# Kernel tuning notes

Measured on AMD Instinct MI355X. Metric: run time of the kernel, lower is better.

The kernel has to match this reference:

```python
import jax, jax.numpy as jnp
import numpy as np

NUM_ITEMS = 50000
EMBED = 256
HEADS = 8
HEAD_DIM = EMBED // HEADS
B, S = 32, 512
NEG_BIG = -1e9   # mask fill for dot-product scores
NEG_SMALL = -1e5 # mask fill for rel / time maps (as in RKT)


def setup_inputs() -> dict:
    key = jax.random.key(0)
    ks = jax.random.split(key, 20)
    sc = 0.02
    return {
        "item_inputs": jax.random.randint(ks[0], (B, S), 0, NUM_ITEMS + 1),
        "label_inputs": jax.random.randint(ks[1], (B, S), 0, 2, dtype=jnp.int32),
        "item_ids": jax.random.randint(ks[2], (B, S), 0, NUM_ITEMS + 1),
        "rel": jax.random.uniform(ks[3], (B, S, S), jnp.float32),
        "timestamp": jax.random.uniform(ks[4], (B, S, S), jnp.float32) * 10.0,
        # learned params
        "item_embeds": jax.random.normal(ks[5], (NUM_ITEMS + 1, EMBED), jnp.float32) * sc,
        "W_in": jax.random.normal(ks[6], (2 * EMBED, EMBED), jnp.float32) * sc,
        "b_in": jnp.zeros((EMBED,), jnp.float32),
        "Wq": jax.random.normal(ks[7], (EMBED, EMBED), jnp.float32) * sc,
        "bq": jnp.zeros((EMBED,), jnp.float32),
        "Wk": jax.random.normal(ks[8], (EMBED, EMBED), jnp.float32) * sc,
        "bk": jnp.zeros((EMBED,), jnp.float32),
        "Wv": jax.random.normal(ks[9], (EMBED, EMBED), jnp.float32) * sc,
        "bv": jnp.zeros((EMBED,), jnp.float32),
        "W_out": jax.random.normal(ks[10], (EMBED, 1), jnp.float32) * sc,
        "b_out": jnp.zeros((1,), jnp.float32),
        "l1": jnp.float32(0.5),
        "l2": jnp.float32(0.5),
    }


def _split_heads(t, W, b):
    # [B,S,E] -> [B,H,S,HD]
    return (t @ W + b).reshape(B, S, HEADS, HEAD_DIM).transpose(0, 2, 1, 3)


def reference(item_inputs, label_inputs, item_ids, rel, timestamp, item_embeds,
              W_in, b_in, Wq, bq, Wk, bk, Wv, bv, W_out, b_out, l1, l2):
    # --- input construction: response-gated duplicated item embedding ---
    e = item_embeds[item_inputs]                       # [B,S,E]
    lab = label_inputs[..., None].astype(e.dtype)      # [B,S,1]
    inputs = jnp.concatenate([e * lab, e * (1.0 - lab)], axis=-1)  # [B,S,2E]
    inputs = jax.nn.relu(inputs @ W_in + b_in)         # [B,S,E]
    query = item_embeds[item_ids]                      # [B,S,E]

    future = jnp.triu(jnp.ones((S, S), bool), 1)       # True above diagonal

    Q = _split_heads(query, Wq, bq)
    K = _split_heads(inputs, Wk, bk)
    V = _split_heads(inputs, Wv, bv)

    # scaled dot-product scores with causal mask
    scores = jnp.einsum('bhqd,bhkd->bhqk', Q, K) / np.float32(np.sqrt(HEAD_DIM))
    prob_attn = jax.nn.softmax(jnp.where(future, NEG_BIG, scores), axis=-1)

    # relational (item-item correlation) attention, future-masked
    rel_m = rel * (~future).astype(rel.dtype)          # [B,S,S]
    rel_attn = jax.nn.softmax(jnp.where(rel_m == 0, NEG_SMALL, rel_m), axis=-1)
    rel_attn = rel_attn[:, None]                       # broadcast over heads

    # exponential time-decay attention, future-masked
    ts = jnp.exp(-jnp.abs(timestamp))
    time_attn = jax.nn.softmax(jnp.where(future, NEG_SMALL, ts), axis=-1)[:, None]

    attn = (1.0 - l2) * prob_attn + l2 * time_attn
    attn = (1.0 - l1) * attn + l1 * rel_attn           # [B,H,S,S]

    out = jnp.einsum('bhqk,bhkd->bhqd', attn, V)       # [B,H,S,HD]
    out = out.transpose(0, 2, 1, 3).reshape(B, S, EMBED)
    logits = out @ W_out + b_out                       # [B,S,1]
    return logits, attn
```

## Files before the change

kernel.cpp:

```cpp
#include <hip/hip_runtime.h>
#include <hip/hip_bf16.h>

#define SEQ 512
#define EMB 256
#define NHEAD 8
#define HD 32

using bf16x8 = __attribute__((ext_vector_type(8))) short;
using f32x4  = __attribute__((ext_vector_type(4))) float;

static __device__ __forceinline__ unsigned short f2bf(float x) {
    union { float f; unsigned int u; } v; v.f = x;
    unsigned int r = v.u + 0x7FFFu + ((v.u >> 16) & 1u);
    return (unsigned short)(r >> 16);
}
static __device__ __forceinline__ float bf2f(unsigned short v) {
    union { unsigned int u; float f; } w; w.u = ((unsigned int)v) << 16; return w.f;
}

__global__ __launch_bounds__(256) void fused_prep_kernel(
    const int* __restrict__ item_inputs,
    const int* __restrict__ label_inputs,
    const int* __restrict__ item_ids,
    const float* __restrict__ embeds,
    const float* __restrict__ W_in,
    const float* __restrict__ Wq,
    const float* __restrict__ Wk,
    const float* __restrict__ Wv,
    const float* __restrict__ Wout,
    const float* __restrict__ bv,
    const float* __restrict__ bout,
    const float* __restrict__ rel,
    const float* __restrict__ tsp,
    unsigned short* __restrict__ Abig,
    unsigned short* __restrict__ qbf,
    unsigned short* __restrict__ WTin,
    unsigned short* __restrict__ WTq,
    unsigned short* __restrict__ WTk,
    float* __restrict__ Wvw,
    float* __restrict__ bvw,
    float* __restrict__ logits,
    float* __restrict__ denp,
    float* __restrict__ dent,
    float* __restrict__ denr)
{
    const int bid = blockIdx.x;
    const int t = threadIdx.x;

    if (bid < 4096) {
        int r = bid * 4 + (t >> 6);
        int j = (t & 63) * 4;
        int item = item_inputs[r];
        int lab  = label_inputs[r];
        int qid  = item_ids[r];
        float4 e4 = *(const float4*)(embeds + (size_t)item * EMB + j);
        ushort4 on  = make_ushort4(f2bf(e4.x), f2bf(e4.y), f2bf(e4.z), f2bf(e4.w));
        ushort4 off = make_ushort4(0, 0, 0, 0);
        *(ushort4*)(Abig + (size_t)r * 512 + j)       = lab ? on : off;
        *(ushort4*)(Abig + (size_t)r * 512 + 256 + j) = lab ? off : on;
        float4 q4 = *(const float4*)(embeds + (size_t)qid * EMB + j);
        *(ushort4*)(qbf + (size_t)r * 256 + j) =
            make_ushort4(f2bf(q4.x), f2bf(q4.y), f2bf(q4.z), f2bf(q4.w));
    } else if (bid < 5705) {
        int idx = (bid - 4096) * 256 + t;
        if (idx < 131072) {
            int n = idx >> 9, k = idx & 511;
            WTin[idx] = f2bf(W_in[(size_t)k * 256 + n]);
        } else if (idx < 196608) {
            int i = idx - 131072;
            int n = i >> 8, k = i & 255;
            WTq[i] = f2bf(Wq[(size_t)k * 256 + n]);
        } else if (idx < 262144) {
            int i = idx - 196608;
            int n = i >> 8, k = i & 255;
            WTk[i] = f2bf(Wk[(size_t)k * 256 + n]);
        } else if (idx < 264192) {
            int i = idx - 262144;
            int c = i >> 3, h = i & 7;
            float s = 0.f;
            #pragma unroll
            for (int d = 0; d < 32; d++)
                s += Wv[(size_t)c * 256 + h * 32 + d] * Wout[h * 32 + d];
            Wvw[i] = s;
        } else if (idx < 264200) {
            int h = idx - 264192;
            float s = 0.f;
            #pragma unroll
            for (int d = 0; d < 32; d++) s += bv[h * 32 + d] * Wout[h * 32 + d];
            bvw[h] = s;
        } else if (idx < 280584) {
            logits[idx - 264200] = bout[0];
        } else if (idx < 411656) {
            denp[idx - 280584] = 0.f;
        }
    } else {
        const int id2 = bid - 5705;
        const int b = id2 >> 4;
        const int qt = id2 & 15;
        const int q0 = qt * 32;
        const int row = t >> 3;
        const int lane8 = t & 7;
        const int qrow = q0 + row;
        const size_t base = ((size_t)(b * SEQ) + qrow) * SEQ;
        float dt = 0.f, dr = 0.f;
        for (int k4 = lane8 * 4; k4 <= qrow; k4 += 32) {
            float4 tv4 = *(const float4*)(tsp + base + k4);
            float4 rv4 = *(const float4*)(rel + base + k4);
            const float* tvp = &tv4.x;
            const float* rvp = &rv4.x;
            #pragma unroll
            for (int j = 0; j < 4; j++) {
                const bool va = (k4 + j) <= qrow;
                dt += va ? __expf(__expf(-fabsf(tvp[j]))) : 0.f;
                dr += (va && rvp[j] != 0.f) ? __expf(rvp[j]) : 0.f;
            }
        }
        dt += __shfl_xor(dt, 1); dt += __shfl_xor(dt, 2); dt += __shfl_xor(dt, 4);
        dr += __shfl_xor(dr, 1); dr += __shfl_xor(dr, 2); dr += __shfl_xor(dr, 4);
        if (lane8 == 0) {
            dent[b * SEQ + qrow] = dt;
            denr[b * SEQ + qrow] = dr;
        }
    }
}

template<int KDIM, int RELU, int OUTBF>
static __device__ __forceinline__ void gemm_body(
    const unsigned short* __restrict__ A,
    const unsigned short* __restrict__ BT,
    const float* __restrict__ bias,
    void* __restrict__ Cout, float scale)
{
    __shared__ unsigned short As[64][40];
    __shared__ unsigned short Bs[128][40];
    const int t = threadIdx.x;
    const int row0 = blockIdx.x * 64;
    const int col0 = blockIdx.y * 128;
    const int wid = t >> 6, lane = t & 63;
    const int wm = wid & 1, wn = wid >> 1;
    const int lg = lane >> 4, l15 = lane & 15;

    f32x4 acc[2][4];
    #pragma unroll
    for (int i = 0; i < 2; i++)
        #pragma unroll
        for (int j = 0; j < 4; j++) acc[i][j] = (f32x4){0.f, 0.f, 0.f, 0.f};

    const int arow = t >> 2, achk = t & 3;
    const int brow = t >> 1, bhalf = t & 1;

    for (int k0 = 0; k0 < KDIM; k0 += 32) {
        __syncthreads();
        *(uint4*)(&As[arow][achk * 8]) =
            *(const uint4*)(A + (size_t)(row0 + arow) * KDIM + k0 + achk * 8);
        const unsigned short* bsrc = BT + (size_t)(col0 + brow) * KDIM + k0 + bhalf * 16;
        *(uint4*)(&Bs[brow][bhalf * 16])     = *(const uint4*)(bsrc);
        *(uint4*)(&Bs[brow][bhalf * 16 + 8]) = *(const uint4*)(bsrc + 8);
        __syncthreads();
        bf16x8 af[2], bfr[4];
        #pragma unroll
        for (int fm = 0; fm < 2; fm++)
            af[fm] = *(const bf16x8*)(&As[wm * 32 + fm * 16 + l15][lg * 8]);
        #pragma unroll
        for (int fn = 0; fn < 4; fn++)
            bfr[fn] = *(const bf16x8*)(&Bs[wn * 64 + fn * 16 + l15][lg * 8]);
        #pragma unroll
        for (int fm = 0; fm < 2; fm++)
            #pragma unroll
            for (int fn = 0; fn < 4; fn++)
                acc[fm][fn] = __builtin_amdgcn_mfma_f32_16x16x32_bf16(
                    af[fm], bfr[fn], acc[fm][fn], 0, 0, 0);
    }
    #pragma unroll
    for (int fm = 0; fm < 2; fm++)
        #pragma unroll
        for (int fn = 0; fn < 4; fn++) {
            int col = col0 + wn * 64 + fn * 16 + l15;
            float bvv = bias[col];
            #pragma unroll
            for (int r = 0; r < 4; r++) {
                int row = row0 + wm * 32 + fm * 16 + lg * 4 + r;
                float v = acc[fm][fn][r] + bvv;
                if (RELU) v = fmaxf(v, 0.f);
                v *= scale;
                if (OUTBF) ((unsigned short*)Cout)[(size_t)row * 256 + col] = f2bf(v);
                else       ((float*)Cout)[(size_t)row * 256 + col] = v;
            }
        }
}

__global__ __launch_bounds__(256, 2) void gemmA_kernel(
    const unsigned short* __restrict__ Abig,
    const unsigned short* __restrict__ WTin,
    const float* __restrict__ b_in,
    unsigned short* __restrict__ Xbf,
    const unsigned short* __restrict__ qbf,
    const unsigned short* __restrict__ WTq,
    const float* __restrict__ bq,
    unsigned short* __restrict__ Qbf)
{
    if (blockIdx.z == 0)
        gemm_body<512, 1, 1>(Abig, WTin, b_in, (void*)Xbf, 1.0f);
    else
        gemm_body<256, 0, 1>(qbf, WTq, bq, (void*)Qbf, 0.17677669529663687f);
}

static __device__ __forceinline__ void vw_body(
    const unsigned short* __restrict__ Xbf,
    const float* __restrict__ Wvw,
    const float* __restrict__ bvw,
    float* __restrict__ Vw)
{
    __shared__ float sW[2048];
    __shared__ float sb[8];
    int t = threadIdx.x;
    #pragma unroll
    for (int i = 0; i < 8; i++) sW[i * 256 + t] = Wvw[i * 256 + t];
    if (t < 8) sb[t] = bvw[t];
    __syncthreads();
    int row = blockIdx.x * 256 + t;
    float acc[8];
    #pragma unroll
    for (int h = 0; h < 8; h++) acc[h] = sb[h];
    for (int d0 = 0; d0 < 32; d0++) {
        bf16x8 x = *(const bf16x8*)(Xbf + (size_t)row * 256 + d0 * 8);
        #pragma unroll
        for (int j = 0; j < 8; j++) {
            float xf = bf2f((unsigned short)x[j]);
            #pragma unroll
            for (int h = 0; h < 8; h++) acc[h] += xf * sW[(d0 * 8 + j) * 8 + h];
        }
    }
    *(float4*)(Vw + (size_t)row * 8)     = make_float4(acc[0], acc[1], acc[2], acc[3]);
    *(float4*)(Vw + (size_t)row * 8 + 4) = make_float4(acc[4], acc[5], acc[6], acc[7]);
}

__global__ __launch_bounds__(256, 2) void gemmB_kernel(
    const unsigned short* __restrict__ Xbf,
    const unsigned short* __restrict__ WTk,
    const float* __restrict__ bk,
    unsigned short* __restrict__ Kbf,
    const float* __restrict__ Wvw,
    const float* __restrict__ bvw,
    float* __restrict__ Vw)
{
    if (blockIdx.z == 0) {
        gemm_body<256, 0, 1>(Xbf, WTk, bk, (void*)Kbf, 1.0f);
    } else {
        if (blockIdx.x >= 64 || blockIdx.y != 0) return;
        vw_body(Xbf, Wvw, bvw, Vw);
    }
}

__global__ __launch_bounds__(256, 8) void attnDp_kernel(
    const unsigned short* __restrict__ Qbf,
    const unsigned short* __restrict__ Kbf,
    float* __restrict__ denp)
{
    const int t = threadIdx.x;
    const int id = blockIdx.x;
    const int b  = id >> 6;
    const int qt = (id >> 2) & 15;
    const int kc = id & 3;
    const int q0 = qt * 32;
    const int w = t >> 6, lane = t & 63;
    const int l15 = lane & 15, lg = lane >> 4;

    bf16x8 aq[2][2];
    #pragma unroll
    for (int hh = 0; hh < 2; hh++)
        #pragma unroll
        for (int mf = 0; mf < 2; mf++)
            aq[hh][mf] = *(const bf16x8*)(Qbf +
                (size_t)(b * SEQ + q0 + mf * 16 + l15) * EMB + (2 * w + hh) * 32 + lg * 8);

    float dp[2][2][4] = {};
    #pragma unroll 1
    for (int i = 0; i < 4; i++) {
        const int kt = kc + 4 * i;
        if (kt > qt) break;
        const int k0 = kt * 32;
        #pragma unroll
        for (int hh = 0; hh < 2; hh++) {
            #pragma unroll
            for (int nf = 0; nf < 2; nf++) {
                bf16x8 bk = *(const bf16x8*)(Kbf +
                    (size_t)(b * SEQ + k0 + nf * 16 + l15) * EMB + (2 * w + hh) * 32 + lg * 8);
                const int kcol = k0 + nf * 16 + l15;
                #pragma unroll
                for (int mf = 0; mf < 2; mf++) {
                    f32x4 am = __builtin_amdgcn_mfma_f32_16x16x32_bf16(
                        aq[hh][mf], bk, (f32x4){0, 0, 0, 0}, 0, 0, 0);
                    #pragma unroll
                    for (int r = 0; r < 4; r++) {
                        const int qrow = q0 + mf * 16 + lg * 4 + r;
                        dp[hh][mf][r] += (kcol <= qrow) ? __expf(am[r]) : 0.f;
                    }
                }
            }
        }
    }

    #pragma unroll
    for (int hh = 0; hh < 2; hh++)
        #pragma unroll
        for (int mf = 0; mf < 2; mf++)
            #pragma unroll
            for (int r = 0; r < 4; r++) {
                float v = dp[hh][mf][r];
                v += __shfl_xor(v, 1); v += __shfl_xor(v, 2);
                v += __shfl_xor(v, 4); v += __shfl_xor(v, 8);
                if (l15 == 0)
                    atomicAdd(&denp[((size_t)(b * NHEAD + 2 * w + hh)) * SEQ
                                    + q0 + mf * 16 + lg * 4 + r], v);
            }
}

__global__ __launch_bounds__(256, 8) void attnW_kernel(
    const unsigned short* __restrict__ Qbf,
    const unsigned short* __restrict__ Kbf,
    const float* __restrict__ Vw,
    const float* __restrict__ rel,
    const float* __restrict__ tsp,
    const float* __restrict__ denp,
    const float* __restrict__ dent,
    const float* __restrict__ denr,
    const float* __restrict__ pl1,
    const float* __restrict__ pl2,
    float* __restrict__ logits,
    float* __restrict__ attn)
{
    __shared__ float sT[16][260];
    __shared__ float slog[4][16];

    const int t = threadIdx.x;
    const int id = blockIdx.x;
    const int qt16 = 31 - (id >> 8);
    const int b = (id >> 3) & 31;
    const int h = id & 7;
    const int q0 = qt16 * 16;
    const int qmax = q0 + 15;

    const int w = t >> 6, lane = t & 63;
    const int l15 = lane & 15, lg = lane >> 4;

    const float l1 = pl1[0], l2 = pl2[0];
    const float cp = (1.f - l1) * (1.f - l2);
    const float ct = (1.f - l1) * l2;
    const float cr = l1;

    const int wrow = t >> 4;
    const int wcol = (t & 15) * 4;
    const int qrow_w = q0 + wrow;
    const float dtv = dent[b * SEQ + qrow_w];
    const float drv = denr[b * SEQ + qrow_w];
    const float ctt = ct / dtv;
    const float crr = drv > 0.f ? cr / drv : 0.f;

    float* arow_base = attn + ((size_t)((b * NHEAD + h) * SEQ) + q0 + wrow) * SEQ;
    const size_t rbase = ((size_t)(b * SEQ) + qrow_w) * SEQ;

    bf16x8 aq = *(const bf16x8*)(Qbf + (size_t)(b * SEQ + q0 + l15) * EMB + h * 32 + lg * 8);

    float invp[4];
    #pragma unroll
    for (int r = 0; r < 4; r++)
        invp[r] = 1.f / denp[((size_t)(b * NHEAD + h)) * SEQ + q0 + lg * 4 + r];

    float plog[4] = {0.f, 0.f, 0.f, 0.f};
    const f32x4 z4 = (f32x4){0.f, 0.f, 0.f, 0.f};

    for (int pass = 0; pass < 2; pass++) {
        const int c0 = pass * 256;
        if (c0 > qmax) {
            #pragma unroll
            for (int s = 0; s < 4; s++) {
                const int cf = wcol + s * 64;
                __builtin_nontemporal_store(z4, (f32x4*)(arow_base + c0 + cf));
            }
            continue;
        }
        #pragma unroll
        for (int s = 0; s < 4; s++) {
            const int cf = wcol + s * 64;
            const int kbase = c0 + cf;
            if (kbase > qrow_w) {
                *(f32x4*)(&sT[wrow][cf]) = z4;
            } else {
                float4 tv4 = *(const float4*)(tsp + rbase + kbase);
                float4 rv4 = *(const float4*)(rel + rbase + kbase);
                const float* tvp = &tv4.x;
                const float* rvp = &rv4.x;
                f32x4 o;
                #pragma unroll
                for (int j = 0; j < 4; j++) {
                    const bool va = (kbase + j) <= qrow_w;
                    float e_t = va ? __expf(__expf(-fabsf(tvp[j]))) * ctt : 0.f;
                    float e_r = (va && rvp[j] != 0.f) ? __expf(rvp[j]) * crr : 0.f;
                    o[j] = e_t + e_r;
                }
                *(f32x4*)(&sT[wrow][cf]) = o;
            }
        }
        __syncthreads();
        #pragma unroll
        for (int ki = 0; ki < 2; ki++) {
            const int kt = w + ki * 4;
            const int k0 = c0 + kt * 32;
            if (k0 <= qmax) {
                #pragma unroll
                for (int nf = 0; nf < 2; nf++) {
                    const int kcol = k0 + nf * 16 + l15;
                    const int lcol = kt * 32 + nf * 16 + l15;
                    bf16x8 bk = *(const bf16x8*)(Kbf +
                        (size_t)(b * SEQ + kcol) * EMB + h * 32 + lg * 8);
                    const float vwv = Vw[(size_t)(b * SEQ + kcol) * 8 + h];
                    f32x4 am = __builtin_amdgcn_mfma_f32_16x16x32_bf16(
                        aq, bk, (f32x4){0.f, 0.f, 0.f, 0.f}, 0, 0, 0);
                    #pragma unroll
                    for (int r = 0; r < 4; r++) {
                        const int qloc = lg * 4 + r;
                        if (kcol <= q0 + qloc) {
                            float a = fmaf(cp * __expf(am[r]), invp[r], sT[qloc][lcol]);
                            sT[qloc][lcol] = a;
                            plog[r] = fmaf(a, vwv, plog[r]);
                        }
                    }
                }
            }
        }
        __syncthreads();
        #pragma unroll
        for (int s = 0; s < 4; s++) {
            const int cf = wcol + s * 64;
            f32x4 v = *(f32x4*)(&sT[wrow][cf]);
            __builtin_nontemporal_store(v, (f32x4*)(arow_base + c0 + cf));
        }
        __syncthreads();
    }

    #pragma unroll
    for (int r = 0; r < 4; r++) {
        float v = plog[r];
        v += __shfl_xor(v, 1); v += __shfl_xor(v, 2);
        v += __shfl_xor(v, 4); v += __shfl_xor(v, 8);
        if (l15 == 0) slog[w][lg * 4 + r] = v;
    }
    __syncthreads();
    if (t < 16)
        atomicAdd(&logits[b * SEQ + q0 + t],
                  slog[0][t] + slog[1][t] + slog[2][t] + slog[3][t]);
}

extern "C" void kernel_launch(void* const* d_in, const int* in_sizes, int n_in,
                              void* d_out, int out_size, void* d_ws, size_t ws_size,
                              hipStream_t stream)
{
    (void)in_sizes; (void)n_in; (void)out_size; (void)ws_size;
    const int*   item_inputs  = (const int*)d_in[0];
    const int*   label_inputs = (const int*)d_in[1];
    const int*   item_ids     = (const int*)d_in[2];
    const float* rel   = (const float*)d_in[3];
    const float* tsp   = (const float*)d_in[4];
    const float* emb   = (const float*)d_in[5];
    const float* W_in  = (const float*)d_in[6];
    const float* b_in  = (const float*)d_in[7];
    const float* Wq    = (const float*)d_in[8];
    const float* bq    = (const float*)d_in[9];
    const float* Wk    = (const float*)d_in[10];
    const float* bk    = (const float*)d_in[11];
    const float* Wv    = (const float*)d_in[12];
    const float* bv    = (const float*)d_in[13];
    const float* Wout  = (const float*)d_in[14];
    const float* bout  = (const float*)d_in[15];
    const float* l1    = (const float*)d_in[16];
    const float* l2    = (const float*)d_in[17];

    const size_t R = 16384;
    char* w = (char*)d_ws;
    unsigned short* Abig = (unsigned short*)w; w += R * 512 * 2;
    unsigned short* qbf  = (unsigned short*)w; w += R * 256 * 2;
    unsigned short* WTin = (unsigned short*)w; w += (size_t)256 * 512 * 2;
    unsigned short* WTq  = (unsigned short*)w; w += (size_t)256 * 256 * 2;
    unsigned short* WTk  = (unsigned short*)w; w += (size_t)256 * 256 * 2;
    unsigned short* Xbf  = (unsigned short*)w; w += R * 256 * 2;
    unsigned short* Qbf  = (unsigned short*)w; w += R * 256 * 2;
    unsigned short* Kbf  = (unsigned short*)w; w += R * 256 * 2;
    float* Wvw  = (float*)w; w += 2048 * 4;
    float* Vw   = (float*)w; w += R * 8 * 4;
    float* bvw  = (float*)w; w += 256;
    float* denp = (float*)w; w += (size_t)32 * NHEAD * SEQ * 4;
    float* dent = (float*)w; w += (size_t)32 * SEQ * 4;
    float* denr = (float*)w; w += (size_t)32 * SEQ * 4;

    float* logits = (float*)d_out;
    float* attnp  = (float*)d_out + 16384;

    fused_prep_kernel<<<dim3(6217), dim3(256), 0, stream>>>(
        item_inputs, label_inputs, item_ids, emb,
        W_in, Wq, Wk, Wv, Wout, bv, bout, rel, tsp,
        Abig, qbf, WTin, WTq, WTk, Wvw, bvw, logits, denp, dent, denr);

    gemmA_kernel<<<dim3(256, 2, 2), dim3(256), 0, stream>>>(
        Abig, WTin, b_in, Xbf, qbf, WTq, bq, Qbf);

    gemmB_kernel<<<dim3(256, 2, 2), dim3(256), 0, stream>>>(
        Xbf, WTk, bk, Kbf, Wvw, bvw, Vw);

    attnDp_kernel<<<dim3(2048), dim3(256), 0, stream>>>(Qbf, Kbf, denp);

    attnW_kernel<<<dim3(8192), dim3(256), 0, stream>>>(
        Qbf, Kbf, Vw, rel, tsp, denp, dent, denr, l1, l2, logits, attnp);
}
```

Baseline: 177.5 us.

## Fuse softmax denominator pass into attention-weight kernel with full-row shared tile

Removes the separate attnDp kernel that computed dot-product softmax denominators with atomics. Each attnW block now computes the exp-scores for its full 16x512 row tile into shared memory, reduces the denominators locally, then does one pass that combines them with the time and rel terms, writes attn and accumulates logits. This drops a launch, the denp zeroing and the atomics, and the second read of Q/K. The cost is a larger shared-memory footprint (~35KB) and a lower occupancy hint (4 blocks instead of 8).

Measured after the change: 153.7 us. -13.4%, faster.

```diff
diff --git a/kernel.cpp b/kernel.cpp
--- a/kernel.cpp
+++ b/kernel.cpp
@@ -40,7 +40,6 @@
     float* __restrict__ Wvw,
     float* __restrict__ bvw,
     float* __restrict__ logits,
-    float* __restrict__ denp,
     float* __restrict__ dent,
     float* __restrict__ denr)
 {
@@ -61,7 +60,7 @@
         float4 q4 = *(const float4*)(embeds + (size_t)qid * EMB + j);
         *(ushort4*)(qbf + (size_t)r * 256 + j) =
             make_ushort4(f2bf(q4.x), f2bf(q4.y), f2bf(q4.z), f2bf(q4.w));
-    } else if (bid < 5705) {
+    } else if (bid < 5193) {
         int idx = (bid - 4096) * 256 + t;
         if (idx < 131072) {
             int n = idx >> 9, k = idx & 511;
@@ -90,11 +89,9 @@
             bvw[h] = s;
         } else if (idx < 280584) {
             logits[idx - 264200] = bout[0];
-        } else if (idx < 411656) {
-            denp[idx - 280584] = 0.f;
         }
     } else {
-        const int id2 = bid - 5705;
+        const int id2 = bid - 5193;
         const int b = id2 >> 4;
         const int qt = id2 & 15;
         const int q0 = qt * 32;
@@ -252,77 +249,12 @@
     }
 }
 
-__global__ __launch_bounds__(256, 8) void attnDp_kernel(
-    const unsigned short* __restrict__ Qbf,
-    const unsigned short* __restrict__ Kbf,
-    float* __restrict__ denp)
-{
-    const int t = threadIdx.x;
-    const int id = blockIdx.x;
-    const int b  = id >> 6;
-    const int qt = (id >> 2) & 15;
-    const int kc = id & 3;
-    const int q0 = qt * 32;
-    const int w = t >> 6, lane = t & 63;
-    const int l15 = lane & 15, lg = lane >> 4;
-
-    bf16x8 aq[2][2];
-    #pragma unroll
-    for (int hh = 0; hh < 2; hh++)
-        #pragma unroll
-        for (int mf = 0; mf < 2; mf++)
-            aq[hh][mf] = *(const bf16x8*)(Qbf +
-                (size_t)(b * SEQ + q0 + mf * 16 + l15) * EMB + (2 * w + hh) * 32 + lg * 8);
-
-    float dp[2][2][4] = {};
-    #pragma unroll 1
-    for (int i = 0; i < 4; i++) {
-        const int kt = kc + 4 * i;
-        if (kt > qt) break;
-        const int k0 = kt * 32;
-        #pragma unroll
-        for (int hh = 0; hh < 2; hh++) {
-            #pragma unroll
-            for (int nf = 0; nf < 2; nf++) {
-                bf16x8 bk = *(const bf16x8*)(Kbf +
-                    (size_t)(b * SEQ + k0 + nf * 16 + l15) * EMB + (2 * w + hh) * 32 + lg * 8);
-                const int kcol = k0 + nf * 16 + l15;
-                #pragma unroll
-                for (int mf = 0; mf < 2; mf++) {
-                    f32x4 am = __builtin_amdgcn_mfma_f32_16x16x32_bf16(
-                        aq[hh][mf], bk, (f32x4){0, 0, 0, 0}, 0, 0, 0);
-                    #pragma unroll
-                    for (int r = 0; r < 4; r++) {
-                        const int qrow = q0 + mf * 16 + lg * 4 + r;
-                        dp[hh][mf][r] += (kcol <= qrow) ? __expf(am[r]) : 0.f;
-                    }
-                }
-            }
-        }
-    }
-
-    #pragma unroll
-    for (int hh = 0; hh < 2; hh++)
-        #pragma unroll
-        for (int mf = 0; mf < 2; mf++)
-            #pragma unroll
-            for (int r = 0; r < 4; r++) {
-                float v = dp[hh][mf][r];
-                v += __shfl_xor(v, 1); v += __shfl_xor(v, 2);
-                v += __shfl_xor(v, 4); v += __shfl_xor(v, 8);
-                if (l15 == 0)
-                    atomicAdd(&denp[((size_t)(b * NHEAD + 2 * w + hh)) * SEQ
-                                    + q0 + mf * 16 + lg * 4 + r], v);
-            }
-}
-
-__global__ __launch_bounds__(256, 8) void attnW_kernel(
+__global__ __launch_bounds__(256, 4) void attnW_kernel(
     const unsigned short* __restrict__ Qbf,
     const unsigned short* __restrict__ Kbf,
     const float* __restrict__ Vw,
     const float* __restrict__ rel,
     const float* __restrict__ tsp,
-    const float* __restrict__ denp,
     const float* __restrict__ dent,
     const float* __restrict__ denr,
     const float* __restrict__ pl1,
@@ -330,8 +262,9 @@
     float* __restrict__ logits,
     float* __restrict__ attn)
 {
-    __shared__ float sT[16][260];
-    __shared__ float slog[4][16];
+    __shared__ float sP[16][516];
+    __shared__ float sVw[512];
+    __shared__ float sden[4][16];
 
     const int t = threadIdx.x;
     const int id = blockIdx.x;
@@ -349,107 +282,94 @@
     const float ct = (1.f - l1) * l2;
     const float cr = l1;
 
+    sVw[t]       = Vw[((size_t)(b * SEQ) + t) * 8 + h];
+    sVw[256 + t] = Vw[((size_t)(b * SEQ) + 256 + t) * 8 + h];
+
+    bf16x8 aq = *(const bf16x8*)(Qbf + (size_t)(b * SEQ + q0 + l15) * EMB + h * 32 + lg * 8);
+
+    float dp[4] = {0.f, 0.f, 0.f, 0.f};
+    #pragma unroll
+    for (int ki = 0; ki < 4; ki++) {
+        const int kt = w + ki * 4;
+        const int k0 = kt * 32;
+        if (k0 <= qmax) {
+            #pragma unroll
+            for (int nf = 0; nf < 2; nf++) {
+                const int kcol = k0 + nf * 16 + l15;
+                const int lcol = k0 + nf * 16 + l15;
+                bf16x8 bk = *(const bf16x8*)(Kbf +
+                    (size_t)(b * SEQ + kcol) * EMB + h * 32 + lg * 8);
+                f32x4 am = __builtin_amdgcn_mfma_f32_16x16x32_bf16(
+                    aq, bk, (f32x4){0.f, 0.f, 0.f, 0.f}, 0, 0, 0);
+                #pragma unroll
+                for (int r = 0; r < 4; r++) {
+                    const int qloc = lg * 4 + r;
+                    float e = (kcol <= q0 + qloc) ? __expf(am[r]) : 0.f;
+                    sP[qloc][lcol] = e;
+                    dp[r] += e;
+                }
+            }
+        } else {
+            #pragma unroll
+            for (int nf = 0; nf < 2; nf++)
+                #pragma unroll
+                for (int r = 0; r < 4; r++)
+                    sP[lg * 4 + r][k0 + nf * 16 + l15] = 0.f;
+        }
+    }
+    #pragma unroll
+    for (int r = 0; r < 4; r++) {
+        float v = dp[r];
+        v += __shfl_xor(v, 1); v += __shfl_xor(v, 2);
+        v += __shfl_xor(v, 4); v += __shfl_xor(v, 8);
+        if (l15 == 0) sden[w][lg * 4 + r] = v;
+    }
+    __syncthreads();
+
     const int wrow = t >> 4;
     const int wcol = (t & 15) * 4;
     const int qrow_w = q0 + wrow;
+    const float den = sden[0][wrow] + sden[1][wrow] + sden[2][wrow] + sden[3][wrow];
+    const float cpinv = cp / den;
     const float dtv = dent[b * SEQ + qrow_w];
     const float drv = denr[b * SEQ + qrow_w];
     const float ctt = ct / dtv;
     const float crr = drv > 0.f ? cr / drv : 0.f;
 
-    float* arow_base = attn + ((size_t)((b * NHEAD + h) * SEQ) + q0 + wrow) * SEQ;
+    float* arow = attn + ((size_t)((b * NHEAD + h) * SEQ) + qrow_w) * SEQ;
     const size_t rbase = ((size_t)(b * SEQ) + qrow_w) * SEQ;
-
-    bf16x8 aq = *(const bf16x8*)(Qbf + (size_t)(b * SEQ + q0 + l15) * EMB + h * 32 + lg * 8);
-
-    float invp[4];
-    #pragma unroll
-    for (int r = 0; r < 4; r++)
-        invp[r] = 1.f / denp[((size_t)(b * NHEAD + h)) * SEQ + q0 + lg * 4 + r];
-
-    float plog[4] = {0.f, 0.f, 0.f, 0.f};
     const f32x4 z4 = (f32x4){0.f, 0.f, 0.f, 0.f};
-
-    for (int pass = 0; pass < 2; pass++) {
-        const int c0 = pass * 256;
-        if (c0 > qmax) {
-            #pragma unroll
-            for (int s = 0; s < 4; s++) {
-                const int cf = wcol + s * 64;
-                __builtin_nontemporal_store(z4, (f32x4*)(arow_base + c0 + cf));
+    float plog = 0.f;
+
+    #pragma unroll
+    for (int s = 0; s < 8; s++) {
+        const int c = wcol + s * 64;
+        f32x4 o;
+        if (c > qrow_w) {
+            o = z4;
+        } else {
+            float4 tv4 = *(const float4*)(tsp + rbase + c);
+            float4 rv4 = *(const float4*)(rel + rbase + c);
+            const float* tvp = &tv4.x;
+            const float* rvp = &rv4.x;
+            #pragma unroll
+            for (int j = 0; j < 4; j++) {
+                const bool va = (c + j) <= qrow_w;
+                float e_t = va ? __expf(__expf(-fabsf(tvp[j]))) * ctt : 0.f;
+                float e_r = (va && rvp[j] != 0.f) ? __expf(rvp[j]) * crr : 0.f;
+                float a = fmaf(sP[wrow][c + j], cpinv, e_t + e_r);
+                a = va ? a : 0.f;
+                o[j] = a;
+                plog = fmaf(a, sVw[c + j], plog);
             }
-            continue;
-        }
-        #pragma unroll
-        for (int s = 0; s < 4; s++) {
-            const int cf = wcol + s * 64;
-            const int kbase = c0 + cf;
-            if (kbase > qrow_w) {
-                *(f32x4*)(&sT[wrow][cf]) = z4;
-            } else {
-                float4 tv4 = *(const float4*)(tsp + rbase + kbase);
-                float4 rv4 = *(const float4*)(rel + rbase + kbase);
-                const float* tvp = &tv4.x;
-                const float* rvp = &rv4.x;
-                f32x4 o;
-                #pragma unroll
-                for (int j = 0; j < 4; j++) {
-                    const bool va = (kbase + j) <= qrow_w;
-                    float e_t = va ? __expf(__expf(-fabsf(tvp[j]))) * ctt : 0.f;
-                    float e_r = (va && rvp[j] != 0.f) ? __expf(rvp[j]) * crr : 0.f;
-                    o[j] = e_t + e_r;
-                }
-                *(f32x4*)(&sT[wrow][cf]) = o;
-            }
-        }
-        __syncthreads();
-        #pragma unroll
-        for (int ki = 0; ki < 2; ki++) {
-            const int kt = w + ki * 4;
-            const int k0 = c0 + kt * 32;
-            if (k0 <= qmax) {
-                #pragma unroll
-                for (int nf = 0; nf < 2; nf++) {
-                    const int kcol = k0 + nf * 16 + l15;
-                    const int lcol = kt * 32 + nf * 16 + l15;
-                    bf16x8 bk = *(const bf16x8*)(Kbf +
-                        (size_t)(b * SEQ + kcol) * EMB + h * 32 + lg * 8);
-                    const float vwv = Vw[(size_t)(b * SEQ + kcol) * 8 + h];
-                    f32x4 am = __builtin_amdgcn_mfma_f32_16x16x32_bf16(
-                        aq, bk, (f32x4){0.f, 0.f, 0.f, 0.f}, 0, 0, 0);
-                    #pragma unroll
-                    for (int r = 0; r < 4; r++) {
-                        const int qloc = lg * 4 + r;
-                        if (kcol <= q0 + qloc) {
-                            float a = fmaf(cp * __expf(am[r]), invp[r], sT[qloc][lcol]);
-                            sT[qloc][lcol] = a;
-                            plog[r] = fmaf(a, vwv, plog[r]);
-                        }
-                    }
-                }
-            }
-        }
-        __syncthreads();
-        #pragma unroll
-        for (int s = 0; s < 4; s++) {
-            const int cf = wcol + s * 64;
-            f32x4 v = *(f32x4*)(&sT[wrow][cf]);
-            __builtin_nontemporal_store(v, (f32x4*)(arow_base + c0 + cf));
-        }
-        __syncthreads();
-    }
-
-    #pragma unroll
-    for (int r = 0; r < 4; r++) {
-        float v = plog[r];
-        v += __shfl_xor(v, 1); v += __shfl_xor(v, 2);
-        v += __shfl_xor(v, 4); v += __shfl_xor(v, 8);
-        if (l15 == 0) slog[w][lg * 4 + r] = v;
-    }
-    __syncthreads();
-    if (t < 16)
-        atomicAdd(&logits[b * SEQ + q0 + t],
-                  slog[0][t] + slog[1][t] + slog[2][t] + slog[3][t]);
+        }
+        __builtin_nontemporal_store(o, (f32x4*)(arow + c));
+    }
+
+    plog += __shfl_xor(plog, 1); plog += __shfl_xor(plog, 2);
+    plog += __shfl_xor(plog, 4); plog += __shfl_xor(plog, 8);
+    if ((t & 15) == 0)
+        atomicAdd(&logits[b * SEQ + qrow_w], plog);
 }
 
 extern "C" void kernel_launch(void* const* d_in, const int* in_sizes, int n_in,
@@ -489,17 +409,16 @@
     float* Wvw  = (float*)w; w += 2048 * 4;
     float* Vw   = (float*)w; w += R * 8 * 4;
     float* bvw  = (float*)w; w += 256;
-    float* denp = (float*)w; w += (size_t)32 * NHEAD * SEQ * 4;
     float* dent = (float*)w; w += (size_t)32 * SEQ * 4;
     float* denr = (float*)w; w += (size_t)32 * SEQ * 4;
 
     float* logits = (float*)d_out;
     float* attnp  = (float*)d_out + 16384;
 
-    fused_prep_kernel<<<dim3(6217), dim3(256), 0, stream>>>(
+    fused_prep_kernel<<<dim3(5705), dim3(256), 0, stream>>>(
         item_inputs, label_inputs, item_ids, emb,
         W_in, Wq, Wk, Wv, Wout, bv, bout, rel, tsp,
-        Abig, qbf, WTin, WTq, WTk, Wvw, bvw, logits, denp, dent, denr);
+        Abig, qbf, WTin, WTq, WTk, Wvw, bvw, logits, dent, denr);
 
     gemmA_kernel<<<dim3(256, 2, 2), dim3(256), 0, stream>>>(
         Abig, WTin, b_in, Xbf, qbf, WTq, bq, Qbf);
@@ -507,8 +426,6 @@
     gemmB_kernel<<<dim3(256, 2, 2), dim3(256), 0, stream>>>(
         Xbf, WTk, bk, Kbf, Wvw, bvw, Vw);
 
-    attnDp_kernel<<<dim3(2048), dim3(256), 0, stream>>>(Qbf, Kbf, denp);
-
     attnW_kernel<<<dim3(8192), dim3(256), 0, stream>>>(
-        Qbf, Kbf, Vw, rel, tsp, denp, dent, denr, l1, l2, logits, attnp);
-}
+        Qbf, Kbf, Vw, rel, tsp, dent, denr, l1, l2, logits, attnp);
+}
```
